# Kernel optimization log

Hardware: AMD Instinct MI355X
Metric: run time of the kernel (lower is better)

Reference implementation:

```python
import jax, jax.numpy as jnp
import numpy as np

B, T, H = 4, 2048, 2048


def setup_inputs() -> dict:
    key = jax.random.key(0)
    ks = jax.random.split(key, 10)
    s = 0.02  # weight init scale
    return {
        "hidden": jax.random.normal(ks[0], (B, T, H), jnp.float32),
        "time_decay": jax.random.normal(ks[1], (H,), jnp.float32),
        "time_first": jax.random.normal(ks[2], (H,), jnp.float32),
        "time_mix_key": jax.random.uniform(ks[3], (1, 1, H), jnp.float32),
        "time_mix_value": jax.random.uniform(ks[4], (1, 1, H), jnp.float32),
        "time_mix_receptance": jax.random.uniform(ks[5], (1, 1, H), jnp.float32),
        "Wk": jax.random.normal(ks[6], (H, H), jnp.float32) * s,
        "Wv": jax.random.normal(ks[7], (H, H), jnp.float32) * s,
        "Wr": jax.random.normal(ks[8], (H, H), jnp.float32) * s,
        "Wo": jax.random.normal(ks[9], (H, H), jnp.float32) * s,
    }


def _wkv(time_decay, time_first, k, v):
    # k, v: [B, T, D]. Log-sum-exp stabilized RWKV WKV recurrence via lax.scan.
    td = -jnp.exp(time_decay.astype(jnp.float32))  # [D]
    tf = time_first.astype(jnp.float32)            # [D]
    kT = jnp.swapaxes(k, 0, 1).astype(jnp.float32)  # [T, B, D]
    vT = jnp.swapaxes(v, 0, 1).astype(jnp.float32)
    bd = (k.shape[0], k.shape[2])
    init = (jnp.zeros(bd, jnp.float32),               # num_state
            jnp.zeros(bd, jnp.float32),               # den_state
            jnp.full(bd, -1e38, jnp.float32))         # max_state

    def step(carry, kv_t):
        num, den, mx = carry
        kt, vt = kv_t
        # output for this step
        mfo = jnp.maximum(mx, kt + tf)
        e1 = jnp.exp(mx - mfo)
        e2 = jnp.exp(kt + tf - mfo)
        out = (e1 * num + e2 * vt) / (e1 * den + e2)
        # state update with decay
        mfs = jnp.maximum(mx + td, kt)
        e1s = jnp.exp(mx + td - mfs)
        e2s = jnp.exp(kt - mfs)
        return (e1s * num + e2s * vt, e1s * den + e2s, mfs), out

    _, outT = jax.lax.scan(step, init, (kT, vT))  # [T, B, D]
    return jnp.swapaxes(outT, 0, 1).astype(k.dtype)


def reference(hidden, time_decay, time_first, time_mix_key, time_mix_value,
              time_mix_receptance, Wk, Wv, Wr, Wo):
    # time-shift: shifted[:, t] = hidden[:, t-1], zero at t=0
    shifted = jnp.pad(hidden, ((0, 0), (1, 0), (0, 0)))[:, :-1]
    key = hidden * time_mix_key + shifted * (1.0 - time_mix_key)
    value = hidden * time_mix_value + shifted * (1.0 - time_mix_value)
    rec = hidden * time_mix_receptance + shifted * (1.0 - time_mix_receptance)
    k = key @ Wk
    v = value @ Wv
    r = jax.nn.sigmoid(rec @ Wr)
    rwkv = _wkv(time_decay, time_first, k, v)
    return (r * rwkv) @ Wo
```

## Files before the change

kernel.cpp:

```cpp
#include <hip/hip_runtime.h>
#include <hip/hip_bf16.h>
#include <stdint.h>


typedef short short8 __attribute__((ext_vector_type(8)));
typedef float f32x4 __attribute__((ext_vector_type(4)));

#define WKV_C 32

__device__ __forceinline__ void gld_lds16(const void* gptr, void* lptr) {
  void* g = const_cast<void*>(gptr);
  __builtin_amdgcn_global_load_lds(
      (__attribute__((address_space(1))) void*)g,
      (__attribute__((address_space(3))) void*)lptr, 16, 0, 0);
}

__device__ __forceinline__ unsigned short f2bf(float f) {
  __bf16 b = (__bf16)f;
  return __builtin_bit_cast(unsigned short, b);
}
__device__ __forceinline__ unsigned short f2h(float f) {
  _Float16 h = (_Float16)f;
  return __builtin_bit_cast(unsigned short, h);
}
__device__ __forceinline__ float h2f(unsigned short u) {
  return (float)__builtin_bit_cast(_Float16, u);
}

__global__ void transpose_cast(const float* __restrict__ W,
                               unsigned short* __restrict__ WT, int n) {
  __shared__ float tile[32][33];
  const int tx = threadIdx.x, ty = threadIdx.y;
  const int x = blockIdx.x * 32 + tx;
#pragma unroll
  for (int j = 0; j < 32; j += 8) {
    int row = blockIdx.y * 32 + ty + j;
    tile[ty + j][tx] = W[(size_t)row * n + x];
  }
  __syncthreads();
#pragma unroll
  for (int j = 0; j < 32; j += 8) {
    int orow = blockIdx.x * 32 + ty + j;
    int ocol = blockIdx.y * 32 + tx;
    WT[(size_t)orow * n + ocol] = f2bf(tile[tx][ty + j]);
  }
}

__global__ void mix3_kernel(const float4* __restrict__ hid,
                            const float4* __restrict__ mk4,
                            const float4* __restrict__ mv4,
                            const float4* __restrict__ mr4,
                            ushort4* __restrict__ xk, ushort4* __restrict__ xv,
                            ushort4* __restrict__ xr, int T, int H4) {
  size_t idx = (size_t)blockIdx.x * blockDim.x + threadIdx.x;
  int c4 = (int)(idx % H4);
  int t = (int)(idx / H4) % T;
  float4 h = hid[idx];
  float4 p = make_float4(0.f, 0.f, 0.f, 0.f);
  if (t != 0) p = hid[idx - H4];
  float4 mk = mk4[c4], mv = mv4[c4], mr = mr4[c4];
  ushort4 ok, ov, orr;
  ok.x = f2bf(h.x * mk.x + p.x * (1.f - mk.x));
  ok.y = f2bf(h.y * mk.y + p.y * (1.f - mk.y));
  ok.z = f2bf(h.z * mk.z + p.z * (1.f - mk.z));
  ok.w = f2bf(h.w * mk.w + p.w * (1.f - mk.w));
  ov.x = f2bf(h.x * mv.x + p.x * (1.f - mv.x));
  ov.y = f2bf(h.y * mv.y + p.y * (1.f - mv.y));
  ov.z = f2bf(h.z * mv.z + p.z * (1.f - mv.z));
  ov.w = f2bf(h.w * mv.w + p.w * (1.f - mv.w));
  orr.x = f2bf(h.x * mr.x + p.x * (1.f - mr.x));
  orr.y = f2bf(h.y * mr.y + p.y * (1.f - mr.y));
  orr.z = f2bf(h.z * mr.z + p.z * (1.f - mr.z));
  orr.w = f2bf(h.w * mr.w + p.w * (1.f - mr.w));
  xk[idx] = ok;
  xv[idx] = ov;
  xr[idx] = orr;
}

#define MODE_F32 0
#define MODE_F16 1
#define MODE_F16_SIG 2

__global__ __launch_bounds__(256) void gemm_bt(
    const unsigned short* __restrict__ A, const unsigned short* __restrict__ Bt,
    void* __restrict__ Cv, int N, int K, int mode) {
  __shared__ unsigned short lta[128 * 64];
  __shared__ unsigned short ltb[128 * 64];

  const int tid = threadIdx.x;
  const int lane = tid & 63;
  const int wave = tid >> 6;
  const int wm = wave >> 1, wn = wave & 1;
  const int quad = lane >> 4, lm = lane & 15;
  const int sw = lm & 7;

  const int lin = blockIdx.y * 16 + blockIdx.x;
  const int cls = lin & 7;
  const int q = lin >> 3;
  const int mTile = cls * 8 + (q & 7);
  const int nTile = q >> 3;
  const int mBase = mTile * 128;
  const int nBase = nTile * 128;

  const unsigned short* AgS[4];
  const unsigned short* BgS[4];
  unsigned short* LaS[4];
  unsigned short* LbS[4];
#pragma unroll
  for (int j = 0; j < 4; ++j) {
    int c = tid + j * 256;
    int row = c >> 3;
    int kb = (c & 7) ^ (row & 7);
    AgS[j] = A + (size_t)(mBase + row) * K + kb * 8;
    BgS[j] = Bt + (size_t)(nBase + row) * K + kb * 8;
    LaS[j] = lta + c * 8;
    LbS[j] = ltb + c * 8;
  }

  const unsigned short* lap[2][4];
  const unsigned short* lbp[2][4];
#pragma unroll
  for (int kk = 0; kk < 2; ++kk)
#pragma unroll
    for (int i = 0; i < 4; ++i) {
      int chA = (kk * 4 + quad) ^ sw;
      lap[kk][i] = lta + (wm * 64 + i * 16 + lm) * 64 + chA * 8;
      lbp[kk][i] = ltb + (wn * 64 + i * 16 + lm) * 64 + chA * 8;
    }

  f32x4 acc[4][4];
#pragma unroll
  for (int i = 0; i < 4; ++i)
#pragma unroll
    for (int j = 0; j < 4; ++j) {
      f32x4 zz = {0.f, 0.f, 0.f, 0.f};
      acc[i][j] = zz;
    }

  for (int k0 = 0; k0 < K; k0 += 64) {
    __syncthreads();
#pragma unroll
    for (int j = 0; j < 4; ++j) gld_lds16(AgS[j] + k0, LaS[j]);
#pragma unroll
    for (int j = 0; j < 4; ++j) gld_lds16(BgS[j] + k0, LbS[j]);
    __syncthreads();
#pragma unroll
    for (int kk = 0; kk < 2; ++kk) {
      short8 aF[4], bF[4];
#pragma unroll
      for (int i = 0; i < 4; ++i) aF[i] = *(const short8*)lap[kk][i];
#pragma unroll
      for (int j = 0; j < 4; ++j) bF[j] = *(const short8*)lbp[kk][j];
#pragma unroll
      for (int i = 0; i < 4; ++i)
#pragma unroll
        for (int j = 0; j < 4; ++j)
          acc[i][j] = __builtin_amdgcn_mfma_f32_16x16x32_bf16(
              aF[i], bF[j], acc[i][j], 0, 0, 0);
    }
  }

#pragma unroll
  for (int i = 0; i < 4; ++i) {
#pragma unroll
    for (int j = 0; j < 4; ++j) {
      const int r0 = mBase + wm * 64 + i * 16 + quad * 4;
      const int cc = nBase + wn * 64 + j * 16 + lm;
#pragma unroll
      for (int rg = 0; rg < 4; ++rg) {
        float x = acc[i][j][rg];
        size_t off = (size_t)(r0 + rg) * N + cc;
        if (mode == MODE_F32) {
          ((float*)Cv)[off] = x;
        } else {
          if (mode == MODE_F16_SIG) x = 1.0f / (1.0f + __expf(-x));
          ((unsigned short*)Cv)[off] = f2h(x);
        }
      }
    }
  }
}

__global__ void wkv_pass1(const unsigned short* __restrict__ kk,
                          const unsigned short* __restrict__ vv,
                          const float* __restrict__ tdec,
                          float* __restrict__ pn, float* __restrict__ pd,
                          float* __restrict__ pm, int T, int H, int L) {
  int idx = blockIdx.x * blockDim.x + threadIdx.x;
  int h = idx % H;
  int bc = idx / H;
  int c = bc % WKV_C;
  int b = bc / WKV_C;
  const float td = -__expf(tdec[h]);
  size_t base = ((size_t)b * T + (size_t)c * L) * H + h;
  const unsigned short* kp = kk + base;
  const unsigned short* vp = vv + base;
  float num = 0.f, den = 0.f, mx = -1e38f;
#pragma unroll 8
  for (int t = 0; t < L; ++t) {
    float kt = h2f(kp[(size_t)t * H]);
    float vt = h2f(vp[(size_t)t * H]);
    float mtd = mx + td;
    float mfs = fmaxf(mtd, kt);
    float e1s = __expf(mtd - mfs);
    float e2s = __expf(kt - mfs);
    num = e1s * num + e2s * vt;
    den = e1s * den + e2s;
    mx = mfs;
  }
  pn[idx] = num;
  pd[idx] = den;
  pm[idx] = mx;
}

__global__ void wkv_pass2(const float* __restrict__ pn,
                          const float* __restrict__ pd,
                          const float* __restrict__ pm,
                          const float* __restrict__ tdec,
                          float* __restrict__ sn, float* __restrict__ sd,
                          float* __restrict__ sm, int H, int L) {
  int idx = blockIdx.x * blockDim.x + threadIdx.x;
  int h = idx % H;
  int b = idx / H;
  const float Ltd = -__expf(tdec[h]) * (float)L;
  float num = 0.f, den = 0.f, mx = -1e38f;
#pragma unroll
  for (int c = 0; c < WKV_C; ++c) {
    size_t o = ((size_t)b * WKV_C + c) * H + h;
    sn[o] = num;
    sd[o] = den;
    sm[o] = mx;
    float mtd = mx + Ltd;
    float cm = pm[o];
    float mnew = fmaxf(mtd, cm);
    float e1 = __expf(mtd - mnew);
    float e2 = __expf(cm - mnew);
    num = e1 * num + e2 * pn[o];
    den = e1 * den + e2 * pd[o];
    mx = mnew;
  }
}

__global__ void wkv_pass3(const unsigned short* __restrict__ kk,
                          const unsigned short* __restrict__ vv,
                          const unsigned short* rr,
                          const float* __restrict__ sn,
                          const float* __restrict__ sd,
                          const float* __restrict__ sm,
                          const float* __restrict__ tdec,
                          const float* __restrict__ tfir, unsigned short* y,
                          int T, int H, int L) {
  int idx = blockIdx.x * blockDim.x + threadIdx.x;
  int h = idx % H;
  int bc = idx / H;
  int c = bc % WKV_C;
  int b = bc / WKV_C;
  const float td = -__expf(tdec[h]);
  const float tf = tfir[h];
  float num = sn[idx], den = sd[idx], mx = sm[idx];
  size_t base = ((size_t)b * T + (size_t)c * L) * H + h;
  const unsigned short* kp = kk + base;
  const unsigned short* vp = vv + base;
  const unsigned short* rp = rr + base;
  unsigned short* yp = y + base;
#pragma unroll 4
  for (int t = 0; t < L; ++t) {
    size_t o = (size_t)t * H;
    float kt = h2f(kp[o]);
    float vt = h2f(vp[o]);
    float rt = h2f(rp[o]);
    float ktf = kt + tf;
    float mfo = fmaxf(mx, ktf);
    float e1 = __expf(mx - mfo);
    float e2 = __expf(ktf - mfo);
    float out = __fdividef(e1 * num + e2 * vt, e1 * den + e2);
    yp[o] = f2bf(rt * out);
    float mtd = mx + td;
    float mfs = fmaxf(mtd, kt);
    float e1s = __expf(mtd - mfs);
    float e2s = __expf(kt - mfs);
    num = e1s * num + e2s * vt;
    den = e1s * den + e2s;
    mx = mfs;
  }
}

extern "C" void kernel_launch(void* const* d_in, const int* in_sizes, int n_in,
                              void* d_out, int out_size, void* d_ws,
                              size_t ws_size, hipStream_t stream) {
  const int Bb = 4, T = 2048, H = 2048;
  const int M = Bb * T;
  const int L = T / WKV_C;

  const float* hidden = (const float*)d_in[0];
  const float* time_decay = (const float*)d_in[1];
  const float* time_first = (const float*)d_in[2];
  const float* tmk = (const float*)d_in[3];
  const float* tmv = (const float*)d_in[4];
  const float* tmr = (const float*)d_in[5];
  const float* Wk = (const float*)d_in[6];
  const float* Wv = (const float*)d_in[7];
  const float* Wr = (const float*)d_in[8];
  const float* Wo = (const float*)d_in[9];
  float* out = (float*)d_out;

  const size_t szWT = (size_t)H * H * 2;
  const size_t szMH = (size_t)M * H * 2;
  const size_t need = szWT + 4 * szMH + 1024;
  if (ws_size < need) return;

  char* ws = (char*)d_ws;
  size_t off = 0;
  auto alloc = [&](size_t bytes) {
    char* p = ws + off;
    off += (bytes + 255) & ~(size_t)255;
    return p;
  };
  unsigned short* WT = (unsigned short*)alloc(szWT);
  unsigned short* A1 = (unsigned short*)alloc(szMH);
  unsigned short* A2 = (unsigned short*)alloc(szMH);
  unsigned short* A3 = (unsigned short*)alloc(szMH);
  unsigned short* A4 = (unsigned short*)alloc(szMH);

  unsigned short* xk = A1;
  unsigned short* xv = A2;
  unsigned short* xr = A3;
  unsigned short* kbuf = A4;
  unsigned short* vbuf = A1;
  unsigned short* rbuf = A2;

  const size_t nCH = (size_t)Bb * WKV_C * H;
  float* pn = (float*)A3;
  float* pd = pn + nCH;
  float* pm = pd + nCH;
  float* sn = pm + nCH;
  float* sd = sn + nCH;
  float* sm = sd + nCH;

  const dim3 txG(H / 32, H / 32), txB(32, 8);
  const int H4 = H / 4;
  const dim3 gmG(H / 128, M / 128), gmB(256);

  mix3_kernel<<<dim3((M * H4) / 256), dim3(256), 0, stream>>>(
      (const float4*)hidden, (const float4*)tmk, (const float4*)tmv,
      (const float4*)tmr, (ushort4*)xk, (ushort4*)xv, (ushort4*)xr, T, H4);

  transpose_cast<<<txG, txB, 0, stream>>>(Wk, WT, H);
  gemm_bt<<<gmG, gmB, 0, stream>>>(xk, WT, kbuf, H, H, MODE_F16);
  transpose_cast<<<txG, txB, 0, stream>>>(Wv, WT, H);
  gemm_bt<<<gmG, gmB, 0, stream>>>(xv, WT, vbuf, H, H, MODE_F16);
  transpose_cast<<<txG, txB, 0, stream>>>(Wr, WT, H);
  gemm_bt<<<gmG, gmB, 0, stream>>>(xr, WT, rbuf, H, H, MODE_F16_SIG);

  const int nThreads1 = Bb * WKV_C * H;
  wkv_pass1<<<dim3(nThreads1 / 256), dim3(256), 0, stream>>>(
      kbuf, vbuf, time_decay, pn, pd, pm, T, H, L);
  wkv_pass2<<<dim3((Bb * H) / 256), dim3(256), 0, stream>>>(
      pn, pd, pm, time_decay, sn, sd, sm, H, L);
  wkv_pass3<<<dim3(nThreads1 / 256), dim3(256), 0, stream>>>(
      kbuf, vbuf, rbuf, sn, sd, sm, time_decay, time_first, rbuf, T, H, L);

  transpose_cast<<<txG, txB, 0, stream>>>(Wo, WT, H);
  gemm_bt<<<gmG, gmB, 0, stream>>>(rbuf, WT, out, H, H, MODE_F32);
}
```

Before: 593.6 us.

## Rewrite bf16 GEMM as 256x256-tile, 8-wave, double-buffered ping-pong pipeline

Replaces the 128x128 single-buffered GEMM with a 256x256 tile computed by 512 threads (8 waves), with double-buffered LDS staging through global_load_lds. The loop is split into phases that interleave async global-to-LDS prefetch of future K-tiles with MFMA work, using explicit vmcnt waits, barriers and setprio. This is meant to hide global-load latency and raise data reuse per tile. In exchange it uses 128 KB of LDS and many more accumulator registers, and it assumes K is a multiple of 128 and dimensions divisible by 256.

```diff
diff --git a/kernel.cpp b/kernel.cpp
--- a/kernel.cpp
+++ b/kernel.cpp
@@ -81,95 +81,157 @@
 #define MODE_F16 1
 #define MODE_F16_SIG 2
 
-__global__ __launch_bounds__(256) void gemm_bt(
+#define STAGE_A(kt_, u, b)                                                     \
+  {                                                                            \
+    _Pragma("unroll") for (int s_ = 0; s_ < 2; ++s_)                           \
+        gld_lds16(A + (mBase + s_ * 128 + (u) * 64) * K +                      \
+                      (size_t)(kt_) * 64 + aLaneOff,                           \
+                  &ldsm[(b) * 16384 + (s_ * 128 + (u) * 64) * 64 + t * 8]);    \
+  }
+#define STAGE_B(kt_, u, b)                                                     \
+  {                                                                            \
+    _Pragma("unroll") for (int s_ = 0; s_ < 2; ++s_)                           \
+        gld_lds16(Bt + (nBase + s_ * 128 + (u) * 32) * K +                     \
+                      (size_t)(kt_) * 64 + bLaneOff,                           \
+                  &ldsm[32768 + (b) * 16384 + ((u) * 128 + s_ * 64) * 64 +     \
+                        t * 8]);                                               \
+  }
+
+#define LOAD_A(b, qi)                                                          \
+  {                                                                            \
+    _Pragma("unroll") for (int ip_ = 0; ip_ < 4; ++ip_) {                      \
+      aF[ip_][0] =                                                             \
+          *(const short8*)(pA0 + (b) * 16384 + (qi) * 4096 + ip_ * 1024);      \
+      aF[ip_][1] =                                                             \
+          *(const short8*)(pA1 + (b) * 16384 + (qi) * 4096 + ip_ * 1024);      \
+    }                                                                          \
+  }
+#define LOAD_B(b, qj, dst)                                                     \
+  {                                                                            \
+    _Pragma("unroll") for (int jj_ = 0; jj_ < 2; ++jj_) {                      \
+      dst[jj_][0] =                                                            \
+          *(const short8*)(pB0 + (b) * 16384 + (qj) * 8192 + jj_ * 1024);      \
+      dst[jj_][1] =                                                            \
+          *(const short8*)(pB1 + (b) * 16384 + (qj) * 8192 + jj_ * 1024);      \
+    }                                                                          \
+  }
+
+#define MFMA16(qi, qj, bfr)                                                    \
+  {                                                                            \
+    _Pragma("unroll") for (int ip_ = 0; ip_ < 4; ++ip_)                        \
+        _Pragma("unroll") for (int jj_ = 0; jj_ < 2; ++jj_) {                  \
+      acc[(qi) * 4 + ip_][(qj) * 2 + jj_] =                                    \
+          __builtin_amdgcn_mfma_f32_16x16x32_bf16(                             \
+              aF[ip_][0], bfr[jj_][0], acc[(qi) * 4 + ip_][(qj) * 2 + jj_],    \
+              0, 0, 0);                                                        \
+      acc[(qi) * 4 + ip_][(qj) * 2 + jj_] =                                    \
+          __builtin_amdgcn_mfma_f32_16x16x32_bf16(                             \
+              aF[ip_][1], bfr[jj_][1], acc[(qi) * 4 + ip_][(qj) * 2 + jj_],    \
+              0, 0, 0);                                                        \
+    }                                                                          \
+  }
+
+#define PHASE(b, qi, qj, STG, WAITN)                                           \
+  {                                                                            \
+    if ((qi) == 0 && (qj) == 0) { LOAD_A(b, 0); LOAD_B(b, 0, bF0); }           \
+    if ((qi) == 0 && (qj) == 1) { LOAD_B(b, 1, bF1); }                         \
+    if ((qi) == 1 && (qj) == 0) { LOAD_A(b, 1); }                              \
+    STG;                                                                       \
+    __builtin_amdgcn_s_barrier();                                              \
+    if ((WAITN) == 6) asm volatile("s_waitcnt vmcnt(6)" ::: "memory");         \
+    if ((WAITN) == 0) asm volatile("s_waitcnt vmcnt(0)" ::: "memory");         \
+    asm volatile("s_waitcnt lgkmcnt(0)" ::: "memory");                         \
+    __builtin_amdgcn_sched_barrier(0);                                         \
+    __builtin_amdgcn_s_setprio(1);                                             \
+    if ((qj) == 0) { MFMA16(qi, 0, bF0); } else { MFMA16(qi, 1, bF1); }        \
+    __builtin_amdgcn_s_setprio(0);                                             \
+    __builtin_amdgcn_s_barrier();                                              \
+  }
+
+#define ITER(kt, LAST)                                                         \
+  {                                                                            \
+    PHASE(0, 0, 0, STAGE_A((kt) + 1, 1, 1), -1);                               \
+    PHASE(0, 0, 1, if (!(LAST)) STAGE_A((kt) + 2, 0, 0), -1);                  \
+    PHASE(0, 1, 0, if (!(LAST)) STAGE_B((kt) + 2, 0, 0), -1);                  \
+    PHASE(0, 1, 1, if (!(LAST)) STAGE_B((kt) + 2, 1, 0), (LAST) ? 0 : 6);      \
+    PHASE(1, 0, 0, if (!(LAST)) STAGE_A((kt) + 2, 1, 0), -1);                  \
+    PHASE(1, 0, 1, if (!(LAST)) STAGE_A((kt) + 3, 0, 1), -1);                  \
+    PHASE(1, 1, 0, if (!(LAST)) STAGE_B((kt) + 3, 0, 1), -1);                  \
+    PHASE(1, 1, 1, if (!(LAST)) STAGE_B((kt) + 3, 1, 1), (LAST) ? -1 : 6);     \
+  }
+
+__global__ __launch_bounds__(512, 2) void gemm_bt(
     const unsigned short* __restrict__ A, const unsigned short* __restrict__ Bt,
     void* __restrict__ Cv, int N, int K, int mode) {
-  __shared__ unsigned short lta[128 * 64];
-  __shared__ unsigned short ltb[128 * 64];
-
-  const int tid = threadIdx.x;
-  const int lane = tid & 63;
-  const int wave = tid >> 6;
-  const int wm = wave >> 1, wn = wave & 1;
-  const int quad = lane >> 4, lm = lane & 15;
+  __shared__ unsigned short ldsm[65536];
+
+  const int t = threadIdx.x;
+  const int lane = t & 63;
+  const int wave = t >> 6;
+  const int wm = wave >> 2;
+  const int wn = wave & 3;
+  const int quad = lane >> 4;
+  const int lm = lane & 15;
   const int sw = lm & 7;
 
-  const int lin = blockIdx.y * 16 + blockIdx.x;
+  const int lin = blockIdx.y * 8 + blockIdx.x;
   const int cls = lin & 7;
   const int q = lin >> 3;
-  const int mTile = cls * 8 + (q & 7);
-  const int nTile = q >> 3;
-  const int mBase = mTile * 128;
-  const int nBase = nTile * 128;
-
-  const unsigned short* AgS[4];
-  const unsigned short* BgS[4];
-  unsigned short* LaS[4];
-  unsigned short* LbS[4];
-#pragma unroll
-  for (int j = 0; j < 4; ++j) {
-    int c = tid + j * 256;
-    int row = c >> 3;
-    int kb = (c & 7) ^ (row & 7);
-    AgS[j] = A + (size_t)(mBase + row) * K + kb * 8;
-    BgS[j] = Bt + (size_t)(nBase + row) * K + kb * 8;
-    LaS[j] = lta + c * 8;
-    LbS[j] = ltb + c * 8;
-  }
-
-  const unsigned short* lap[2][4];
-  const unsigned short* lbp[2][4];
-#pragma unroll
-  for (int kk = 0; kk < 2; ++kk)
-#pragma unroll
-    for (int i = 0; i < 4; ++i) {
-      int chA = (kk * 4 + quad) ^ sw;
-      lap[kk][i] = lta + (wm * 64 + i * 16 + lm) * 64 + chA * 8;
-      lbp[kk][i] = ltb + (wn * 64 + i * 16 + lm) * 64 + chA * 8;
-    }
-
-  f32x4 acc[4][4];
-#pragma unroll
-  for (int i = 0; i < 4; ++i)
+  const int mTile = cls * 4 + (q & 3);
+  const int nTile = q >> 2;
+  const size_t mBase = (size_t)mTile * 256;
+  const size_t nBase = (size_t)nTile * 256;
+
+  const int lr = t >> 3;
+  const int swz = (t & 7) ^ (lr & 7);
+  const int aLaneOff = lr * K + swz * 8;
+  const int bLaneOff = (lr >> 5) * 64 * K + (lr & 31) * K + swz * 8;
+
+  const unsigned short* pA0 = ldsm + (wm * 128 + lm) * 64 + ((0 + quad) ^ sw) * 8;
+  const unsigned short* pA1 = ldsm + (wm * 128 + lm) * 64 + ((4 + quad) ^ sw) * 8;
+  const unsigned short* pB0 =
+      ldsm + 32768 + (wn * 32 + lm) * 64 + ((0 + quad) ^ sw) * 8;
+  const unsigned short* pB1 =
+      ldsm + 32768 + (wn * 32 + lm) * 64 + ((4 + quad) ^ sw) * 8;
+
+  short8 aF[4][2];
+  short8 bF0[2][2];
+  short8 bF1[2][2];
+  f32x4 acc[8][4];
+#pragma unroll
+  for (int i = 0; i < 8; ++i)
 #pragma unroll
     for (int j = 0; j < 4; ++j) {
       f32x4 zz = {0.f, 0.f, 0.f, 0.f};
       acc[i][j] = zz;
     }
 
-  for (int k0 = 0; k0 < K; k0 += 64) {
-    __syncthreads();
-#pragma unroll
-    for (int j = 0; j < 4; ++j) gld_lds16(AgS[j] + k0, LaS[j]);
-#pragma unroll
-    for (int j = 0; j < 4; ++j) gld_lds16(BgS[j] + k0, LbS[j]);
-    __syncthreads();
-#pragma unroll
-    for (int kk = 0; kk < 2; ++kk) {
-      short8 aF[4], bF[4];
-#pragma unroll
-      for (int i = 0; i < 4; ++i) aF[i] = *(const short8*)lap[kk][i];
-#pragma unroll
-      for (int j = 0; j < 4; ++j) bF[j] = *(const short8*)lbp[kk][j];
-#pragma unroll
-      for (int i = 0; i < 4; ++i)
-#pragma unroll
-        for (int j = 0; j < 4; ++j)
-          acc[i][j] = __builtin_amdgcn_mfma_f32_16x16x32_bf16(
-              aF[i], bF[j], acc[i][j], 0, 0, 0);
-    }
-  }
-
-#pragma unroll
-  for (int i = 0; i < 4; ++i) {
+  STAGE_A(0, 0, 0);
+  STAGE_B(0, 0, 0);
+  STAGE_B(0, 1, 0);
+  STAGE_A(0, 1, 0);
+  STAGE_A(1, 0, 1);
+  STAGE_B(1, 0, 1);
+  STAGE_B(1, 1, 1);
+  asm volatile("s_waitcnt vmcnt(6)" ::: "memory");
+  __builtin_amdgcn_s_barrier();
+
+  const int KT = K >> 6;
+  int kt = 0;
+#pragma unroll 1
+  for (; kt + 2 < KT; kt += 2) { ITER(kt, 0); }
+  ITER(kt, 1);
+
+#pragma unroll
+  for (int i = 0; i < 8; ++i) {
+    const size_t row = mBase + wm * 128 + (i >> 2) * 64 + (i & 3) * 16 + quad * 4;
 #pragma unroll
     for (int j = 0; j < 4; ++j) {
-      const int r0 = mBase + wm * 64 + i * 16 + quad * 4;
-      const int cc = nBase + wn * 64 + j * 16 + lm;
+      const size_t col = nBase + wn * 64 + (j >> 1) * 32 + (j & 1) * 16 + lm;
 #pragma unroll
       for (int rg = 0; rg < 4; ++rg) {
         float x = acc[i][j][rg];
-        size_t off = (size_t)(r0 + rg) * N + cc;
+        size_t off = (row + rg) * N + col;
         if (mode == MODE_F32) {
           ((float*)Cv)[off] = x;
         } else {
@@ -339,7 +401,7 @@
 
   const dim3 txG(H / 32, H / 32), txB(32, 8);
   const int H4 = H / 4;
-  const dim3 gmG(H / 128, M / 128), gmB(256);
+  const dim3 gmG(H / 256, M / 256), gmB(512);
 
   mix3_kernel<<<dim3((M * H4) / 256), dim3(256), 0, stream>>>(
       (const float4*)hidden, (const float4*)tmk, (const float4*)tmv,
```

After: 496.5 us. -16.4%, faster.
